# Kernel tuning notes

Measured on AMD Instinct MI355X. Metric: run time of the kernel, lower is better.

## Reference

```python
import jax, jax.numpy as jnp
import numpy as np

CROP = (7, 7)
CANONICAL = 56.0
MIN_LEVEL, MAX_LEVEL = 0, 4


def _crop_and_resize(feat, boxes, box_idx, ch, cw):
    # feat: [B,H,W,C]; boxes: [N,4] interpreted as (y1,x1,y2,x2) in [0,1]
    # TF tf.image.crop_and_resize bilinear semantics, extrapolation_value=0
    B, H, W, C = feat.shape
    y1, x1, y2, x2 = boxes[:, 0], boxes[:, 1], boxes[:, 2], boxes[:, 3]
    Hf, Wf = float(H - 1), float(W - 1)
    gy = jnp.arange(ch, dtype=boxes.dtype)
    gx = jnp.arange(cw, dtype=boxes.dtype)
    ys = y1[:, None] * Hf + gy[None, :] * ((y2 - y1) * Hf / (ch - 1))[:, None]  # [N,ch]
    xs = x1[:, None] * Wf + gx[None, :] * ((x2 - x1) * Wf / (cw - 1))[:, None]  # [N,cw]
    y0f = jnp.floor(ys)
    x0f = jnp.floor(xs)
    ly = (ys - y0f)[:, :, None, None]  # [N,ch,1,1]
    lx = (xs - x0f)[:, None, :, None]  # [N,1,cw,1]
    y0 = jnp.clip(y0f, 0.0, Hf).astype(jnp.int32)
    y1i = jnp.clip(y0f + 1.0, 0.0, Hf).astype(jnp.int32)
    x0 = jnp.clip(x0f, 0.0, Wf).astype(jnp.int32)
    x1i = jnp.clip(x0f + 1.0, 0.0, Wf).astype(jnp.int32)
    b = box_idx[:, None, None]
    v00 = feat[b, y0[:, :, None], x0[:, None, :]]   # [N,ch,cw,C]
    v01 = feat[b, y0[:, :, None], x1i[:, None, :]]
    v10 = feat[b, y1i[:, :, None], x0[:, None, :]]
    v11 = feat[b, y1i[:, :, None], x1i[:, None, :]]
    top = v00 + lx * (v01 - v00)
    bot = v10 + lx * (v11 - v10)
    val = top + ly * (bot - top)
    ok = ((ys >= 0) & (ys <= Hf))[:, :, None] & ((xs >= 0) & (xs <= Wf))[:, None, :]
    return jnp.where(ok[..., None], val, jnp.zeros((), val.dtype))


def _roi_align(boxes, feats, image_shape):
    B, N, _ = boxes.shape
    # source: x1,y1,x2,y2 = split(boxes); h = y2-y1; w = x2-x1
    h = boxes[..., 3] - boxes[..., 1]
    w = boxes[..., 2] - boxes[..., 0]
    area = (image_shape[0] * image_shape[1]).astype(jnp.float32)
    lvl = jnp.log2(jnp.sqrt(h * w) / (CANONICAL / jnp.sqrt(area)))
    lvl = jnp.clip(jnp.round(lvl).astype(jnp.int32), MIN_LEVEL, MAX_LEVEL)  # [B,N]
    # source passes raw boxes to crop_and_resize (interpreted as y1,x1,y2,x2)
    bf = jax.lax.stop_gradient(boxes.reshape(B * N, 4))
    bidx = jnp.repeat(jnp.arange(B, dtype=jnp.int32), N)
    # crops from every level for every box, then select the assigned level
    crops = jnp.stack([_crop_and_resize(f, bf, bidx, CROP[0], CROP[1]) for f in feats])  # [L,BN,7,7,C]
    sel = (lvl.reshape(B * N) - MIN_LEVEL)[None, :, None, None, None]
    pooled = jnp.take_along_axis(crops, sel, axis=0)[0]  # [BN,7,7,C]
    return pooled.reshape(B, N, CROP[0], CROP[1], feats[0].shape[-1])


def setup_inputs() -> dict:
    key = jax.random.key(0)
    kx, ky, kw, kh, k0, k1, k2, k3, k4 = jax.random.split(key, 9)
    B, N, C = 2, 1000, 256
    cx = jax.random.uniform(kx, (B, N), minval=0.25, maxval=0.75)
    cy = jax.random.uniform(ky, (B, N), minval=0.25, maxval=0.75)
    bw = jax.random.uniform(kw, (B, N), minval=0.02, maxval=0.5)
    bh = jax.random.uniform(kh, (B, N), minval=0.02, maxval=0.5)
    x1 = cx - bw / 2.0
    x2 = cx + bw / 2.0
    y1 = cy - bh / 2.0
    y2 = cy + bh / 2.0
    boxes = jnp.stack([x1, y1, x2, y2], axis=-1).astype(jnp.float32)  # [B,N,4]
    sizes = [256, 128, 64, 32, 16]
    feats = [jax.random.normal(k, (B, s, s, C), dtype=jnp.float32)
             for k, s in zip([k0, k1, k2, k3, k4], sizes)]
    return {
        "boxes": boxes,
        "feat0": feats[0], "feat1": feats[1], "feat2": feats[2],
        "feat3": feats[3], "feat4": feats[4],
        "image_shape": jnp.array([1024, 1024], dtype=jnp.int32),
    }


def reference(boxes, feat0, feat1, feat2, feat3, feat4, image_shape):
    return _roi_align(boxes, [feat0, feat1, feat2, feat3, feat4], image_shape)
```

## Files before the change

kernel.cpp:

```cpp
#include <hip/hip_runtime.h>
#include <math.h>

#define CCH 256
#define CROP 7

__global__ __launch_bounds__(64) void roi_align_kernel(
    const float4* __restrict__ boxes,
    const float* __restrict__ f0,
    const float* __restrict__ f1,
    const float* __restrict__ f2,
    const float* __restrict__ f3,
    const float* __restrict__ f4,
    const int*  __restrict__ image_shape,
    float* __restrict__ out,
    int N)
{
    const int cell = blockIdx.x;
    const int bn   = blockIdx.y;
    const int c4   = threadIdx.x;
    const int iy   = cell / CROP;
    const int ix   = cell % CROP;
    const int b    = bn / N;

    const float4 box = boxes[bn];
    const float ry1 = box.x;
    const float cx1 = box.y;
    const float ry2 = box.z;
    const float cx2 = box.w;

    const float h = cx2 - cx1;
    const float w = ry2 - ry1;

    const float area  = (float)(image_shape[0] * image_shape[1]);
    const float canon = 56.0f / sqrtf(area);
    const float lvlf  = log2f(sqrtf(h * w) / canon);
    int lvl = (int)rintf(lvlf);
    lvl = lvl < 0 ? 0 : (lvl > 4 ? 4 : lvl);

    const float* f; int s;
    if      (lvl == 0) { f = f0; s = 256; }
    else if (lvl == 1) { f = f1; s = 128; }
    else if (lvl == 2) { f = f2; s = 64;  }
    else if (lvl == 3) { f = f3; s = 32;  }
    else               { f = f4; s = 16;  }

    const float Hf = (float)(s - 1);
    const float Wf = Hf;

    const float ystep = (ry2 - ry1) * Hf / 6.0f;
    const float xstep = (cx2 - cx1) * Wf / 6.0f;
    const float ys = ry1 * Hf + (float)iy * ystep;
    const float xs = cx1 * Wf + (float)ix * xstep;

    const float y0f = floorf(ys);
    const float x0f = floorf(xs);
    const float ly = ys - y0f;
    const float lx = xs - x0f;

    const int y0  = (int)fminf(fmaxf(y0f,        0.0f), Hf);
    const int y1i = (int)fminf(fmaxf(y0f + 1.0f, 0.0f), Hf);
    const int x0  = (int)fminf(fmaxf(x0f,        0.0f), Wf);
    const int x1i = (int)fminf(fmaxf(x0f + 1.0f, 0.0f), Wf);

    const bool ok = (ys >= 0.0f) && (ys <= Hf) && (xs >= 0.0f) && (xs <= Wf);

    const size_t img  = (size_t)b * s * s * CCH;
    const size_t o00  = img + ((size_t)y0  * s + x0 ) * CCH;
    const size_t o01  = img + ((size_t)y0  * s + x1i) * CCH;
    const size_t o10  = img + ((size_t)y1i * s + x0 ) * CCH;
    const size_t o11  = img + ((size_t)y1i * s + x1i) * CCH;

    const float4 v00 = *((const float4*)(f + o00) + c4);
    const float4 v01 = *((const float4*)(f + o01) + c4);
    const float4 v10 = *((const float4*)(f + o10) + c4);
    const float4 v11 = *((const float4*)(f + o11) + c4);

    float4 val;
    {
        float tx = v00.x + lx * (v01.x - v00.x);
        float bx = v10.x + lx * (v11.x - v10.x);
        val.x = tx + ly * (bx - tx);
        float ty = v00.y + lx * (v01.y - v00.y);
        float by = v10.y + lx * (v11.y - v10.y);
        val.y = ty + ly * (by - ty);
        float tz = v00.z + lx * (v01.z - v00.z);
        float bz = v10.z + lx * (v11.z - v10.z);
        val.z = tz + ly * (bz - tz);
        float tw = v00.w + lx * (v01.w - v00.w);
        float bw = v10.w + lx * (v11.w - v10.w);
        val.w = tw + ly * (bw - tw);
    }
    if (!ok) { val.x = 0.0f; val.y = 0.0f; val.z = 0.0f; val.w = 0.0f; }

    float4* optr = (float4*)(out + ((size_t)bn * (CROP * CROP) + cell) * CCH) + c4;
    *optr = val;
}

extern "C" void kernel_launch(void* const* d_in, const int* in_sizes, int n_in,
                              void* d_out, int out_size, void* d_ws, size_t ws_size,
                              hipStream_t stream) {
    const float4* boxes = (const float4*)d_in[0];
    const float*  f0    = (const float*)d_in[1];
    const float*  f1    = (const float*)d_in[2];
    const float*  f2    = (const float*)d_in[3];
    const float*  f3    = (const float*)d_in[4];
    const float*  f4    = (const float*)d_in[5];
    const int*    ishp  = (const int*)d_in[6];
    float*        out   = (float*)d_out;

    const int BN = in_sizes[0] / 4;
    const int B  = in_sizes[1] / (256 * 256 * 256);
    const int N  = BN / B;

    dim3 grid(CROP * CROP, BN);
    roi_align_kernel<<<grid, 64, 0, stream>>>(boxes, f0, f1, f2, f3, f4, ishp, out, N);
}
```

Baseline: 252.4 us.

## Process all crop cells of a box per 256-thread block with nontemporal stores

```diff
diff --git a/kernel.cpp b/kernel.cpp
--- a/kernel.cpp
+++ b/kernel.cpp
@@ -3,8 +3,11 @@
 
 #define CCH 256
 #define CROP 7
+#define NCELL (CROP * CROP)
 
-__global__ __launch_bounds__(64) void roi_align_kernel(
+typedef float vfloat4 __attribute__((ext_vector_type(4)));
+
+__global__ __launch_bounds__(256) void roi_align_kernel(
     const float4* __restrict__ boxes,
     const float* __restrict__ f0,
     const float* __restrict__ f1,
@@ -15,11 +18,9 @@
     float* __restrict__ out,
     int N)
 {
-    const int cell = blockIdx.x;
-    const int bn   = blockIdx.y;
-    const int c4   = threadIdx.x;
-    const int iy   = cell / CROP;
-    const int ix   = cell % CROP;
+    const int bn   = blockIdx.x;
+    const int lane = threadIdx.x & 63;
+    const int wv   = threadIdx.x >> 6;
     const int b    = bn / N;
 
     const float4 box = boxes[bn];
@@ -49,51 +50,53 @@
 
     const float ystep = (ry2 - ry1) * Hf / 6.0f;
     const float xstep = (cx2 - cx1) * Wf / 6.0f;
-    const float ys = ry1 * Hf + (float)iy * ystep;
-    const float xs = cx1 * Wf + (float)ix * xstep;
 
-    const float y0f = floorf(ys);
-    const float x0f = floorf(xs);
-    const float ly = ys - y0f;
-    const float lx = xs - x0f;
+    const size_t img = (size_t)b * s * s * CCH;
+    vfloat4* outb = (vfloat4*)(out + (size_t)bn * NCELL * CCH);
 
-    const int y0  = (int)fminf(fmaxf(y0f,        0.0f), Hf);
-    const int y1i = (int)fminf(fmaxf(y0f + 1.0f, 0.0f), Hf);
-    const int x0  = (int)fminf(fmaxf(x0f,        0.0f), Wf);
-    const int x1i = (int)fminf(fmaxf(x0f + 1.0f, 0.0f), Wf);
+    for (int cell = wv; cell < NCELL; cell += 4) {
+        const int iy = cell / CROP;
+        const int ix = cell - iy * CROP;
 
-    const bool ok = (ys >= 0.0f) && (ys <= Hf) && (xs >= 0.0f) && (xs <= Wf);
+        const float ys = ry1 * Hf + (float)iy * ystep;
+        const float xs = cx1 * Wf + (float)ix * xstep;
 
-    const size_t img  = (size_t)b * s * s * CCH;
-    const size_t o00  = img + ((size_t)y0  * s + x0 ) * CCH;
-    const size_t o01  = img + ((size_t)y0  * s + x1i) * CCH;
-    const size_t o10  = img + ((size_t)y1i * s + x0 ) * CCH;
-    const size_t o11  = img + ((size_t)y1i * s + x1i) * CCH;
+        const float y0f = floorf(ys);
+        const float x0f = floorf(xs);
+        const float ly = ys - y0f;
+        const float lx = xs - x0f;
 
-    const float4 v00 = *((const float4*)(f + o00) + c4);
-    const float4 v01 = *((const float4*)(f + o01) + c4);
-    const float4 v10 = *((const float4*)(f + o10) + c4);
-    const float4 v11 = *((const float4*)(f + o11) + c4);
+        const int y0  = (int)fminf(fmaxf(y0f,        0.0f), Hf);
+        const int y1i = (int)fminf(fmaxf(y0f + 1.0f, 0.0f), Hf);
+        const int x0  = (int)fminf(fmaxf(x0f,        0.0f), Wf);
+        const int x1i = (int)fminf(fmaxf(x0f + 1.0f, 0.0f), Wf);
 
-    float4 val;
-    {
-        float tx = v00.x + lx * (v01.x - v00.x);
-        float bx = v10.x + lx * (v11.x - v10.x);
-        val.x = tx + ly * (bx - tx);
-        float ty = v00.y + lx * (v01.y - v00.y);
-        float by = v10.y + lx * (v11.y - v10.y);
-        val.y = ty + ly * (by - ty);
-        float tz = v00.z + lx * (v01.z - v00.z);
-        float bz = v10.z + lx * (v11.z - v10.z);
-        val.z = tz + ly * (bz - tz);
-        float tw = v00.w + lx * (v01.w - v00.w);
-        float bw = v10.w + lx * (v11.w - v10.w);
-        val.w = tw + ly * (bw - tw);
+        const bool ok = (ys >= 0.0f) && (ys <= Hf) && (xs >= 0.0f) && (xs <= Wf);
+
+        const float4 v00 = *((const float4*)(f + img + ((size_t)y0  * s + x0 ) * CCH) + lane);
+        const float4 v01 = *((const float4*)(f + img + ((size_t)y0  * s + x1i) * CCH) + lane);
+        const float4 v10 = *((const float4*)(f + img + ((size_t)y1i * s + x0 ) * CCH) + lane);
+        const float4 v11 = *((const float4*)(f + img + ((size_t)y1i * s + x1i) * CCH) + lane);
+
+        vfloat4 val;
+        {
+            float tx = v00.x + lx * (v01.x - v00.x);
+            float bx = v10.x + lx * (v11.x - v10.x);
+            val.x = tx + ly * (bx - tx);
+            float ty = v00.y + lx * (v01.y - v00.y);
+            float by = v10.y + lx * (v11.y - v10.y);
+            val.y = ty + ly * (by - ty);
+            float tz = v00.z + lx * (v01.z - v00.z);
+            float bz = v10.z + lx * (v11.z - v10.z);
+            val.z = tz + ly * (bz - tz);
+            float tw = v00.w + lx * (v01.w - v00.w);
+            float bw = v10.w + lx * (v11.w - v10.w);
+            val.w = tw + ly * (bw - tw);
+        }
+        if (!ok) { val.x = 0.0f; val.y = 0.0f; val.z = 0.0f; val.w = 0.0f; }
+
+        __builtin_nontemporal_store(val, outb + (size_t)cell * 64 + lane);
     }
-    if (!ok) { val.x = 0.0f; val.y = 0.0f; val.z = 0.0f; val.w = 0.0f; }
-
-    float4* optr = (float4*)(out + ((size_t)bn * (CROP * CROP) + cell) * CCH) + c4;
-    *optr = val;
 }
 
 extern "C" void kernel_launch(void* const* d_in, const int* in_sizes, int n_in,
@@ -112,6 +115,5 @@
     const int B  = in_sizes[1] / (256 * 256 * 256);
     const int N  = BN / B;
 
-    dim3 grid(CROP * CROP, BN);
-    roi_align_kernel<<<grid, 64, 0, stream>>>(boxes, f0, f1, f2, f3, f4, ishp, out, N);
+    roi_align_kernel<<<BN, 256, 0, stream>>>(boxes, f0, f1, f2, f3, f4, ishp, out, N);
 }
```

Measured after the change: 262.1 us. 1.04x slower.
